# Performance work log

Measured on AMD Instinct MI355X. Metric: run time of the kernel, lower is better.

The kernel has to match this reference:

```python
import jax, jax.numpy as jnp
import numpy as np
from jax import lax
from jax.scipy.special import logsumexp

B, S, V, D, DFF, H, T, L = 64, 512, 30000, 128, 256, 4, 9, 2
HD = D // H


def setup_inputs() -> dict:
    key = jax.random.key(0)
    ks = jax.random.split(key, 12)
    sc = 0.02
    return {
        "sentences": jax.random.randint(ks[0], (B, S), 0, V, dtype=jnp.int32),
        "tags": jax.random.randint(ks[1], (B, S), 0, T, dtype=jnp.int32),
        "emb": jax.random.normal(ks[2], (V, D), jnp.float32) * sc,
        "Wqkv": jax.random.normal(ks[3], (L, 3 * D, D), jnp.float32) * sc,
        "bqkv": jnp.zeros((L, 3 * D), jnp.float32),
        "Wo": jax.random.normal(ks[4], (L, D, D), jnp.float32) * sc,
        "bo": jnp.zeros((L, D), jnp.float32),
        "W1": jax.random.normal(ks[5], (L, DFF, D), jnp.float32) * sc,
        "b1f": jnp.zeros((L, DFF), jnp.float32),
        "W2": jax.random.normal(ks[6], (L, D, DFF), jnp.float32) * sc,
        "b2f": jnp.zeros((L, D), jnp.float32),
        "ln1g": jnp.ones((L, D), jnp.float32), "ln1b": jnp.zeros((L, D), jnp.float32),
        "ln2g": jnp.ones((L, D), jnp.float32), "ln2b": jnp.zeros((L, D), jnp.float32),
        "Wtag": jax.random.normal(ks[7], (T, D), jnp.float32) * sc,
        "btag": jnp.zeros((T,), jnp.float32),
        "trans": jax.random.normal(ks[8], (T, T), jnp.float32) * 0.1,
        "start_t": jax.random.normal(ks[9], (T,), jnp.float32),
        "end_t": jax.random.normal(ks[10], (T,), jnp.float32),
    }


def _layernorm(x, g, b, eps=1e-5):
    mu = x.mean(-1, keepdims=True)
    var = ((x - mu) ** 2).mean(-1, keepdims=True)
    return (x - mu) / jnp.sqrt(var + eps) * g + b


def _forward_core(sentences, tags, emb, Wqkv, bqkv, Wo, bo, W1, b1f, W2, b2f,
                  ln1g, ln1b, ln2g, ln2b, Wtag, btag, trans, start_t, end_t):
    emb = emb.at[0].set(0.0)  # padding_idx=0
    mask = sentences != 0  # (B,S) key-padding mask (True = real token)
    x = emb[sentences]  # (B,S,D)
    # sinusoidal positional encoding (eval mode -> dropout is identity)
    pos = jnp.arange(S, dtype=jnp.float32)[:, None]
    div = jnp.exp(jnp.arange(0, D, 2, dtype=jnp.float32) * (-np.log(10000.0) / D))
    pe = jnp.zeros((S, D), jnp.float32).at[:, 0::2].set(jnp.sin(pos * div)).at[:, 1::2].set(jnp.cos(pos * div))
    x = x + pe[None]
    key_bias = jnp.where(mask, 0.0, -1e9)[:, None, None, :]  # (B,1,1,S)
    inv_sqrt_hd = 1.0 / np.sqrt(HD)
    for l in range(L):  # post-LN TransformerEncoderLayer, relu FFN
        qkv = x @ Wqkv[l].T + bqkv[l]
        q, k, v = jnp.split(qkv, 3, axis=-1)
        q = q.reshape(B, S, H, HD)
        k = k.reshape(B, S, H, HD)
        v = v.reshape(B, S, H, HD)
        scores = jnp.einsum('bqhd,bkhd->bhqk', q, k) * inv_sqrt_hd + key_bias
        attn = jax.nn.softmax(scores, axis=-1)
        ctx = jnp.einsum('bhqk,bkhd->bqhd', attn, v).reshape(B, S, D)
        x = _layernorm(x + ctx @ Wo[l].T + bo[l], ln1g[l], ln1b[l])
        ff = jax.nn.relu(x @ W1[l].T + b1f[l]) @ W2[l].T + b2f[l]
        x = _layernorm(x + ff, ln2g[l], ln2b[l])
    emissions = x @ Wtag.T + btag  # (B,S,T)

    # CRF forward algorithm (log-partition) as a scan over time
    fv0 = start_t[None, :] + emissions[:, 0]  # (B,T)

    def step(fv, xm):
        em_t, m_t = xm  # (B,T), (B,)
        nv = logsumexp(fv[:, :, None] + trans[None, :, :] + em_t[:, None, :], axis=1)
        return jnp.where(m_t[:, None], nv, fv), None

    fv, _ = lax.scan(step, fv0, (jnp.swapaxes(emissions[:, 1:], 0, 1),
                                 jnp.swapaxes(mask[:, 1:], 0, 1)))
    fwd_score = logsumexp(fv + end_t[None, :], axis=1)  # (B,)

    # gold path score (fully vectorized)
    bidx = jnp.arange(B)
    score = start_t[tags[:, 0]] + emissions[bidx, 0, tags[:, 0]]
    tprev, tcur = tags[:, :-1], tags[:, 1:]
    trans_sc = trans[tprev, tcur]  # (B,S-1)
    emit_sc = jnp.take_along_axis(emissions[:, 1:], tcur[:, :, None], axis=2)[:, :, 0]
    score = score + jnp.sum(jnp.where(mask[:, 1:], trans_sc + emit_sc, 0.0), axis=1)
    seq_lens = mask.sum(axis=1)
    last_tags = tags[bidx, seq_lens - 1]
    score = score + end_t[last_tags]

    return jnp.mean(fwd_score - score)


def reference(sentences, tags, emb, Wqkv, bqkv, Wo, bo, W1, b1f, W2, b2f,
              ln1g, ln1b, ln2g, ln2b, Wtag, btag, trans, start_t, end_t):
    return _forward_core(sentences, tags, emb, Wqkv, bqkv, Wo, bo, W1, b1f, W2, b2f,
                         ln1g, ln1b, ln2g, ln2b, Wtag, btag, trans, start_t, end_t)
```

## Files before the change

kernel.cpp:

```cpp
#include <hip/hip_runtime.h>

#define BB   64
#define SS   512
#define DD   128
#define DFFc 256
#define HH   4
#define TT   9
#define LL   2
#define HDc  32
#define NN   (BB*SS)

#define OFF_X    0
#define OFF_Y    (NN*DD)
#define OFF_QKV  (2*NN*DD)
#define OFF_CTX  (5*NN*DD)
#define OFF_KT   (6*NN*DD)
#define OFF_EM   (7*NN*DD)
#define OFF_PART (7*NN*DD + NN*TT)

typedef __attribute__((ext_vector_type(8))) short short8;
typedef __attribute__((ext_vector_type(8))) unsigned short ushort8;
typedef __attribute__((ext_vector_type(4))) float f32x4;

__device__ __forceinline__ unsigned short f2bf(float f) {
  unsigned int u = __float_as_uint(f);
  u += 0x7FFFu + ((u >> 16) & 1u);
  return (unsigned short)(u >> 16);
}
__device__ __forceinline__ float bf2f(unsigned short h) {
  return __uint_as_float(((unsigned int)h) << 16);
}

__global__ void k_embed(const int* __restrict__ sent, const float* __restrict__ emb,
                        float* __restrict__ x) {
  int n = blockIdx.x;
  int d = threadIdx.x;
  int tok = sent[n];
  int s = n & (SS - 1);
  float e = (tok != 0) ? emb[(size_t)tok * DD + d] : 0.f;
  int i = d >> 1;
  float dv = expf((float)(2 * i) * (-9.210340371976184f / (float)DD));
  float ang = (float)s * dv;
  float pe = (d & 1) ? cosf(ang) : sinf(ang);
  x[(size_t)n * DD + d] = e + pe;
}

template <int KTOT, bool RELU>
__global__ __launch_bounds__(256) void k_gemm(const float* __restrict__ X,
                                              const float* __restrict__ W,
                                              const float* __restrict__ bias,
                                              float* __restrict__ Y, int ldY) {
  __shared__ float Xs[64][68];
  __shared__ float Wt[64][68];
  const int tid = threadIdx.x;
  const int tx = tid & 15, ty = tid >> 4;
  const int n0 = blockIdx.x * 64, c0g = blockIdx.y * 64;
  float acc[4][4] = {};
  for (int kb = 0; kb < KTOT; kb += 64) {
    #pragma unroll
    for (int p = 0; p < 4; p++) {
      int r = p * 16 + (tid >> 4);
      int c4 = (tid & 15) * 4;
      *(float4*)&Xs[r][c4] = *(const float4*)&X[(size_t)(n0 + r) * KTOT + kb + c4];
    }
    #pragma unroll
    for (int p = 0; p < 4; p++) {
      int c = (tid >> 4) + 16 * p;
      int kk0 = tid & 15;
      #pragma unroll
      for (int ii = 0; ii < 4; ii++)
        Wt[kk0 + 16 * ii][c] = W[(size_t)(c0g + c) * KTOT + kb + kk0 + 16 * ii];
    }
    __syncthreads();
    #pragma unroll
    for (int k4 = 0; k4 < 16; k4++) {
      float4 a4[4], b4[4];
      #pragma unroll
      for (int i = 0; i < 4; i++) a4[i] = *(const float4*)&Xs[4 * ty + i][4 * k4];
      #pragma unroll
      for (int k = 0; k < 4; k++) b4[k] = *(const float4*)&Wt[4 * k4 + k][4 * tx];
      #pragma unroll
      for (int k = 0; k < 4; k++) {
        #pragma unroll
        for (int i = 0; i < 4; i++) {
          float av = (k == 0) ? a4[i].x : (k == 1) ? a4[i].y : (k == 2) ? a4[i].z : a4[i].w;
          acc[i][0] = fmaf(av, b4[k].x, acc[i][0]);
          acc[i][1] = fmaf(av, b4[k].y, acc[i][1]);
          acc[i][2] = fmaf(av, b4[k].z, acc[i][2]);
          acc[i][3] = fmaf(av, b4[k].w, acc[i][3]);
        }
      }
    }
    __syncthreads();
  }
  float4 bi = *(const float4*)&bias[c0g + 4 * tx];
  #pragma unroll
  for (int i = 0; i < 4; i++) {
    float4 o;
    o.x = acc[i][0] + bi.x; o.y = acc[i][1] + bi.y;
    o.z = acc[i][2] + bi.z; o.w = acc[i][3] + bi.w;
    if (RELU) {
      o.x = fmaxf(o.x, 0.f); o.y = fmaxf(o.y, 0.f);
      o.z = fmaxf(o.z, 0.f); o.w = fmaxf(o.w, 0.f);
    }
    *(float4*)&Y[(size_t)(n0 + 4 * ty + i) * ldY + c0g + 4 * tx] = o;
  }
}

template <int KTOT>
__global__ __launch_bounds__(256) void k_gemm_ln(const float* __restrict__ X,
                                                 const float* __restrict__ W,
                                                 const float* __restrict__ bias,
                                                 const float* __restrict__ Res,
                                                 const float* __restrict__ gam,
                                                 const float* __restrict__ bet,
                                                 float* __restrict__ Y) {
  __shared__ float Xs[32][68];
  __shared__ float Wt[64][132];
  const int tid = threadIdx.x;
  const int tx = tid & 31, ty = tid >> 5;
  const int n0 = blockIdx.x * 32;
  float acc[4][4] = {};
  for (int kb = 0; kb < KTOT; kb += 64) {
    #pragma unroll
    for (int p = 0; p < 2; p++) {
      int r = p * 16 + (tid >> 4);
      int c4 = (tid & 15) * 4;
      *(float4*)&Xs[r][c4] = *(const float4*)&X[(size_t)(n0 + r) * KTOT + kb + c4];
    }
    #pragma unroll
    for (int p = 0; p < 8; p++) {
      int c = (tid >> 4) + 16 * p;
      int kk0 = tid & 15;
      #pragma unroll
      for (int ii = 0; ii < 4; ii++)
        Wt[kk0 + 16 * ii][c] = W[(size_t)c * KTOT + kb + kk0 + 16 * ii];
    }
    __syncthreads();
    #pragma unroll
    for (int k4 = 0; k4 < 16; k4++) {
      float4 a4[4], b4[4];
      #pragma unroll
      for (int i = 0; i < 4; i++) a4[i] = *(const float4*)&Xs[4 * ty + i][4 * k4];
      #pragma unroll
      for (int k = 0; k < 4; k++) b4[k] = *(const float4*)&Wt[4 * k4 + k][4 * tx];
      #pragma unroll
      for (int k = 0; k < 4; k++) {
        #pragma unroll
        for (int i = 0; i < 4; i++) {
          float av = (k == 0) ? a4[i].x : (k == 1) ? a4[i].y : (k == 2) ? a4[i].z : a4[i].w;
          acc[i][0] = fmaf(av, b4[k].x, acc[i][0]);
          acc[i][1] = fmaf(av, b4[k].y, acc[i][1]);
          acc[i][2] = fmaf(av, b4[k].z, acc[i][2]);
          acc[i][3] = fmaf(av, b4[k].w, acc[i][3]);
        }
      }
    }
    __syncthreads();
  }
  const int c0 = 4 * tx;
  float4 bi = *(const float4*)&bias[c0];
  float4 gm = *(const float4*)&gam[c0];
  float4 be = *(const float4*)&bet[c0];
  #pragma unroll
  for (int i = 0; i < 4; i++) {
    int n = n0 + 4 * ty + i;
    float4 rs = *(const float4*)&Res[(size_t)n * DD + c0];
    float v0 = acc[i][0] + bi.x + rs.x;
    float v1 = acc[i][1] + bi.y + rs.y;
    float v2 = acc[i][2] + bi.z + rs.z;
    float v3 = acc[i][3] + bi.w + rs.w;
    float s1 = v0 + v1 + v2 + v3;
    float s2 = v0 * v0 + v1 * v1 + v2 * v2 + v3 * v3;
    #pragma unroll
    for (int off = 16; off >= 1; off >>= 1) {
      s1 += __shfl_xor(s1, off);
      s2 += __shfl_xor(s2, off);
    }
    float mu = s1 * 0.0078125f;
    float var = s2 * 0.0078125f - mu * mu;
    float rstd = rsqrtf(var + 1e-5f);
    float4 o;
    o.x = (v0 - mu) * rstd * gm.x + be.x;
    o.y = (v1 - mu) * rstd * gm.y + be.y;
    o.z = (v2 - mu) * rstd * gm.z + be.z;
    o.w = (v3 - mu) * rstd * gm.w + be.w;
    *(float4*)&Y[(size_t)n * DD + c0] = o;
  }
}

__global__ void k_pack(const float* __restrict__ qkv,
                       unsigned short* __restrict__ Kh, unsigned short* __restrict__ Kl,
                       unsigned short* __restrict__ Vh, unsigned short* __restrict__ Vl) {
  const int st = blockIdx.x * 64;
  const int bh = blockIdx.y;
  const int b = bh >> 2, h = bh & 3;
  const int tid = threadIdx.x;
  __shared__ float tile[64][33];
  #pragma unroll
  for (int p = 0; p < 8; p++) {
    int sl = p * 8 + (tid >> 5);
    int d = tid & 31;
    const float* src = qkv + (size_t)(b * SS + st + sl) * 384 + h * 32 + d;
    float kv = src[128];
    unsigned short khu = f2bf(kv);
    size_t o = (size_t)(bh * SS + st + sl) * 32 + d;
    Kh[o] = khu;
    Kl[o] = f2bf(kv - bf2f(khu));
    tile[sl][d] = src[256];
  }
  __syncthreads();
  int d = tid >> 3, s0 = (tid & 7) * 8;
  ushort8 vh, vl;
  #pragma unroll
  for (int i = 0; i < 8; i++) {
    float v = tile[s0 + i][d];
    unsigned short hu = f2bf(v);
    vh[i] = hu;
    vl[i] = f2bf(v - bf2f(hu));
  }
  size_t o = (size_t)(bh * 32 + d) * SS + st + s0;
  *(ushort8*)&Vh[o] = vh;
  *(ushort8*)&Vl[o] = vl;
}

__global__ __launch_bounds__(256) void k_attn(const float* __restrict__ qkv,
    const unsigned short* __restrict__ Kh, const unsigned short* __restrict__ Kl,
    const unsigned short* __restrict__ Vh, const unsigned short* __restrict__ Vl,
    const int* __restrict__ sent, float* __restrict__ ctx) {
  const int id = blockIdx.x;
  const int xcd = id & 7, rem = id >> 3;
  const int qt = rem & 7;
  const int bh = xcd + 8 * (rem >> 3);
  const int b = bh >> 2, h = bh & 3;
  const int tid = threadIdx.x, w = tid >> 6, lane = tid & 63;
  const int l15 = lane & 15, kg = lane >> 4;

  __shared__ float kb_lds[512];
  __shared__ unsigned short Ph[4][16][136];
  __shared__ unsigned short Pl[4][16][136];
  __shared__ float l_lds[4][16];

  for (int i = tid; i < 512; i += 256)
    kb_lds[i] = (sent[b * SS + i] != 0) ? 0.f : -1e9f;
  __syncthreads();

  const int qrow = qt * 64 + w * 16 + l15;
  const float* qp = qkv + (size_t)(b * SS + qrow) * 384 + h * 32 + kg * 8;
  short8 qh, ql;
  #pragma unroll
  for (int i = 0; i < 8; i++) {
    float v = qp[i];
    unsigned short hu = f2bf(v);
    qh[i] = (short)hu;
    ql[i] = (short)f2bf(v - bf2f(hu));
  }

  f32x4 acc0 = {0.f, 0.f, 0.f, 0.f};
  f32x4 acc1 = {0.f, 0.f, 0.f, 0.f};
  float ls[4] = {0.f, 0.f, 0.f, 0.f};
  const float scale = 0.17677669529663687f;

  const unsigned short* KhB = Kh + (size_t)bh * SS * 32;
  const unsigned short* KlB = Kl + (size_t)bh * SS * 32;
  const unsigned short* VhB = Vh + (size_t)bh * 32 * SS;
  const unsigned short* VlB = Vl + (size_t)bh * 32 * SS;

  for (int c = 0; c < 4; c++) {
    const int ksb = c * 128;
    f32x4 sc[8];
    #pragma unroll
    for (int t = 0; t < 8; t++) {
      size_t ko = (size_t)(ksb + t * 16 + l15) * 32 + kg * 8;
      short8 kh_ = *(const short8*)(KhB + ko);
      short8 kl_ = *(const short8*)(KlB + ko);
      f32x4 z = {0.f, 0.f, 0.f, 0.f};
      f32x4 s = __builtin_amdgcn_mfma_f32_16x16x32_bf16(qh, kh_, z, 0, 0, 0);
      s = __builtin_amdgcn_mfma_f32_16x16x32_bf16(qh, kl_, s, 0, 0, 0);
      s = __builtin_amdgcn_mfma_f32_16x16x32_bf16(ql, kh_, s, 0, 0, 0);
      sc[t] = s;
    }
    #pragma unroll
    for (int t = 0; t < 8; t++) {
      float kbv = kb_lds[ksb + t * 16 + l15];
      #pragma unroll
      for (int j = 0; j < 4; j++) {
        float s = fmaf(sc[t][j], scale, kbv);
        float p = __expf(s);
        ls[j] += p;
        unsigned short ph = f2bf(p);
        Ph[w][kg * 4 + j][t * 16 + l15] = ph;
        Pl[w][kg * 4 + j][t * 16 + l15] = f2bf(p - bf2f(ph));
      }
    }
    #pragma unroll
    for (int k4 = 0; k4 < 4; k4++) {
      short8 ph_ = *(const short8*)&Ph[w][l15][k4 * 32 + kg * 8];
      short8 pl_ = *(const short8*)&Pl[w][l15][k4 * 32 + kg * 8];
      size_t vo0 = (size_t)l15 * SS + ksb + k4 * 32 + kg * 8;
      size_t vo1 = (size_t)(16 + l15) * SS + ksb + k4 * 32 + kg * 8;
      short8 vh0 = *(const short8*)(VhB + vo0);
      short8 vl0 = *(const short8*)(VlB + vo0);
      acc0 = __builtin_amdgcn_mfma_f32_16x16x32_bf16(vh0, ph_, acc0, 0, 0, 0);
      acc0 = __builtin_amdgcn_mfma_f32_16x16x32_bf16(vh0, pl_, acc0, 0, 0, 0);
      acc0 = __builtin_amdgcn_mfma_f32_16x16x32_bf16(vl0, ph_, acc0, 0, 0, 0);
      short8 vh1 = *(const short8*)(VhB + vo1);
      short8 vl1 = *(const short8*)(VlB + vo1);
      acc1 = __builtin_amdgcn_mfma_f32_16x16x32_bf16(vh1, ph_, acc1, 0, 0, 0);
      acc1 = __builtin_amdgcn_mfma_f32_16x16x32_bf16(vh1, pl_, acc1, 0, 0, 0);
      acc1 = __builtin_amdgcn_mfma_f32_16x16x32_bf16(vl1, ph_, acc1, 0, 0, 0);
    }
  }
  #pragma unroll
  for (int j = 0; j < 4; j++) {
    #pragma unroll
    for (int off = 1; off <= 8; off <<= 1) ls[j] += __shfl_xor(ls[j], off);
  }
  if (l15 == 0) {
    #pragma unroll
    for (int j = 0; j < 4; j++) l_lds[w][kg * 4 + j] = ls[j];
  }
  float linv = 1.f / l_lds[w][l15];
  float* cp = ctx + (size_t)(b * SS + qrow) * DD + h * 32;
  #pragma unroll
  for (int j = 0; j < 4; j++) {
    cp[kg * 4 + j] = acc0[j] * linv;
    cp[16 + kg * 4 + j] = acc1[j] * linv;
  }
}

__global__ void k_emis(const float* __restrict__ X, const float* __restrict__ Wtag,
                       const float* __restrict__ btag, float* __restrict__ em) {
  int idx = blockIdx.x * 256 + threadIdx.x;
  if (idx >= NN * TT) return;
  int n = idx / TT, t = idx - n * TT;
  const float* xr = X + (size_t)n * DD;
  const float* wr = Wtag + (size_t)t * DD;
  float acc = 0.f;
  #pragma unroll
  for (int k = 0; k < DD / 4; k++) {
    float4 x4 = *(const float4*)(xr + 4 * k);
    float4 w4 = *(const float4*)(wr + 4 * k);
    acc += x4.x * w4.x + x4.y * w4.y + x4.z * w4.z + x4.w * w4.w;
  }
  em[idx] = acc + btag[t];
}

__global__ void k_crf_scan(const float* __restrict__ em, const int* __restrict__ sent,
                           const float* __restrict__ trans, float* __restrict__ M) {
  const int i = blockIdx.x;
  const int c = blockIdx.y;
  const int b = blockIdx.z;
  const int lane = threadIdx.x;
  const int j = (lane < TT) ? lane : 0;
  float tr[TT];
  #pragma unroll
  for (int k = 0; k < TT; k++) tr[k] = trans[k * TT + j];
  const float* emb_ = em + (size_t)b * SS * TT;
  float v = (j == i) ? 0.f : -1e30f;
  const int s0 = 1 + c * 64;
  const int s1 = (s0 + 64 < SS) ? s0 + 64 : SS;
  for (int s = s0; s < s1; s++) {
    int tok = sent[b * SS + s];
    if (tok != 0) {
      float a[TT];
      #pragma unroll
      for (int k = 0; k < TT; k++) a[k] = __shfl(v, k) + tr[k];
      float m = a[0];
      #pragma unroll
      for (int k = 1; k < TT; k++) m = fmaxf(m, a[k]);
      float sum = 0.f;
      #pragma unroll
      for (int k = 0; k < TT; k++) sum += __expf(a[k] - m);
      v = emb_[s * TT + j] + m + __logf(sum);
    }
  }
  if (lane < TT) M[(((size_t)b * 8 + c) * TT + i) * TT + j] = v;
}

__global__ void k_crf_comb(const float* __restrict__ em, const int* __restrict__ sent,
                           const int* __restrict__ tags, const float* __restrict__ trans,
                           const float* __restrict__ start_t, const float* __restrict__ end_t,
                           const float* __restrict__ M, float* __restrict__ part) {
  const int b = blockIdx.x;
  const int lane = threadIdx.x;
  const int j = (lane < TT) ? lane : 0;
  const float* emb_ = em + (size_t)b * SS * TT;
  float fv = start_t[j] + emb_[j];
  #pragma unroll
  for (int c = 0; c < 8; c++) {
    const float* Mc = M + (((size_t)b * 8 + c) * TT) * TT;
    float a[TT];
    #pragma unroll
    for (int k = 0; k < TT; k++) a[k] = __shfl(fv, k) + Mc[k * TT + j];
    float m = a[0];
    #pragma unroll
    for (int k = 1; k < TT; k++) m = fmaxf(m, a[k]);
    float sum = 0.f;
    #pragma unroll
    for (int k = 0; k < TT; k++) sum += __expf(a[k] - m);
    fv = m + __logf(sum);
  }
  float aa[TT];
  #pragma unroll
  for (int i = 0; i < TT; i++) aa[i] = __shfl(fv, i) + end_t[i];
  float m2 = aa[0];
  #pragma unroll
  for (int i = 1; i < TT; i++) m2 = fmaxf(m2, aa[i]);
  float sum2 = 0.f;
  #pragma unroll
  for (int i = 0; i < TT; i++) sum2 += __expf(aa[i] - m2);
  float fwd = m2 + __logf(sum2);
  float p = 0.f;
  int cnt = 0;
  #pragma unroll
  for (int ii = 0; ii < 8; ii++) {
    int s = lane + 64 * ii;
    cnt += (sent[b * SS + s] != 0) ? 1 : 0;
    int s2 = s + 1;
    if (s2 < SS && sent[b * SS + s2] != 0) {
      int tp = tags[b * SS + s2 - 1];
      int tc = tags[b * SS + s2];
      p += trans[tp * TT + tc] + emb_[(size_t)s2 * TT + tc];
    }
  }
  #pragma unroll
  for (int off = 32; off >= 1; off >>= 1) {
    p += __shfl_xor(p, off);
    cnt += __shfl_xor(cnt, off);
  }
  if (lane == 0) {
    int t0 = tags[b * SS];
    float score = start_t[t0] + emb_[t0] + p;
    int lastt = tags[b * SS + cnt - 1];
    score += end_t[lastt];
    part[b] = fwd - score;
  }
}

__global__ void k_final(const float* __restrict__ part, float* __restrict__ out) {
  float v = part[threadIdx.x];
  #pragma unroll
  for (int off = 32; off >= 1; off >>= 1) v += __shfl_xor(v, off);
  if (threadIdx.x == 0) out[0] = v * (1.f / 64.f);
}

extern "C" void kernel_launch(void* const* d_in, const int* in_sizes, int n_in,
                              void* d_out, int out_size, void* d_ws, size_t ws_size,
                              hipStream_t stream) {
  const int*   sent  = (const int*)d_in[0];
  const int*   tags  = (const int*)d_in[1];
  const float* emb   = (const float*)d_in[2];
  const float* Wqkv  = (const float*)d_in[3];
  const float* bqkv  = (const float*)d_in[4];
  const float* Wo    = (const float*)d_in[5];
  const float* bo    = (const float*)d_in[6];
  const float* W1    = (const float*)d_in[7];
  const float* b1f   = (const float*)d_in[8];
  const float* W2    = (const float*)d_in[9];
  const float* b2f   = (const float*)d_in[10];
  const float* ln1g  = (const float*)d_in[11];
  const float* ln1b  = (const float*)d_in[12];
  const float* ln2g  = (const float*)d_in[13];
  const float* ln2b  = (const float*)d_in[14];
  const float* Wtag  = (const float*)d_in[15];
  const float* btag  = (const float*)d_in[16];
  const float* trans = (const float*)d_in[17];
  const float* st    = (const float*)d_in[18];
  const float* et    = (const float*)d_in[19];

  float* ws   = (float*)d_ws;
  float* xA   = ws + OFF_X;
  float* xB   = ws + OFF_Y;
  float* qkv  = ws + OFF_QKV;
  float* ff   = ws + OFF_QKV;
  float* ctx  = ws + OFF_CTX;
  float* em   = ws + OFF_EM;
  float* part = ws + OFF_PART;
  float* out  = (float*)d_out;

  unsigned short* Kh = (unsigned short*)(ws + OFF_KT);
  unsigned short* Vh = Kh + (size_t)NN * DD;
  unsigned short* Kl = (unsigned short*)(ws + OFF_Y);
  unsigned short* Vl = Kl + (size_t)NN * DD;
  float* Mbuf = ws + OFF_CTX;

  k_embed<<<NN, DD, 0, stream>>>(sent, emb, xA);

  for (int l = 0; l < LL; l++) {
    k_gemm<128, false><<<dim3(NN / 64, 6), 256, 0, stream>>>(
        xA, Wqkv + (size_t)l * 3 * DD * DD, bqkv + l * 3 * DD, qkv, 3 * DD);
    k_pack<<<dim3(8, BB * HH), 256, 0, stream>>>(qkv, Kh, Kl, Vh, Vl);
    k_attn<<<dim3(2048), 256, 0, stream>>>(qkv, Kh, Kl, Vh, Vl, sent, ctx);
    k_gemm_ln<128><<<dim3(NN / 32), 256, 0, stream>>>(
        ctx, Wo + (size_t)l * DD * DD, bo + l * DD, xA, ln1g + l * DD, ln1b + l * DD, xB);
    k_gemm<128, true><<<dim3(NN / 64, 4), 256, 0, stream>>>(
        xB, W1 + (size_t)l * DFFc * DD, b1f + l * DFFc, ff, DFFc);
    k_gemm_ln<256><<<dim3(NN / 32), 256, 0, stream>>>(
        ff, W2 + (size_t)l * DD * DFFc, b2f + l * DD, xB, ln2g + l * DD, ln2b + l * DD, xA);
  }

  k_emis<<<(NN * TT + 255) / 256, 256, 0, stream>>>(xA, Wtag, btag, em);
  k_crf_scan<<<dim3(TT, 8, BB), 64, 0, stream>>>(em, sent, trans, Mbuf);
  k_crf_comb<<<BB, 64, 0, stream>>>(em, sent, tags, trans, st, et, Mbuf, part);
  k_final<<<1, 64, 0, stream>>>(part, out);
}
```

Baseline: 675.5 us.

## Move dense GEMMs to split-bf16 MFMA with packed hi/lo activations

Result: slower. 735.5 us (+8.9%).

```diff
diff --git a/kernel.cpp b/kernel.cpp
--- a/kernel.cpp
+++ b/kernel.cpp
@@ -32,7 +32,8 @@
 }
 
 __global__ void k_embed(const int* __restrict__ sent, const float* __restrict__ emb,
-                        float* __restrict__ x) {
+                        float* __restrict__ x,
+                        unsigned short* __restrict__ xh, unsigned short* __restrict__ xl) {
   int n = blockIdx.x;
   int d = threadIdx.x;
   int tok = sent[n];
@@ -42,150 +43,144 @@
   float dv = expf((float)(2 * i) * (-9.210340371976184f / (float)DD));
   float ang = (float)s * dv;
   float pe = (d & 1) ? cosf(ang) : sinf(ang);
-  x[(size_t)n * DD + d] = e + pe;
-}
-
-template <int KTOT, bool RELU>
-__global__ __launch_bounds__(256) void k_gemm(const float* __restrict__ X,
-                                              const float* __restrict__ W,
-                                              const float* __restrict__ bias,
-                                              float* __restrict__ Y, int ldY) {
-  __shared__ float Xs[64][68];
-  __shared__ float Wt[64][68];
-  const int tid = threadIdx.x;
-  const int tx = tid & 15, ty = tid >> 4;
-  const int n0 = blockIdx.x * 64, c0g = blockIdx.y * 64;
-  float acc[4][4] = {};
-  for (int kb = 0; kb < KTOT; kb += 64) {
-    #pragma unroll
-    for (int p = 0; p < 4; p++) {
-      int r = p * 16 + (tid >> 4);
-      int c4 = (tid & 15) * 4;
-      *(float4*)&Xs[r][c4] = *(const float4*)&X[(size_t)(n0 + r) * KTOT + kb + c4];
-    }
-    #pragma unroll
-    for (int p = 0; p < 4; p++) {
-      int c = (tid >> 4) + 16 * p;
-      int kk0 = tid & 15;
-      #pragma unroll
-      for (int ii = 0; ii < 4; ii++)
-        Wt[kk0 + 16 * ii][c] = W[(size_t)(c0g + c) * KTOT + kb + kk0 + 16 * ii];
-    }
-    __syncthreads();
-    #pragma unroll
-    for (int k4 = 0; k4 < 16; k4++) {
-      float4 a4[4], b4[4];
-      #pragma unroll
-      for (int i = 0; i < 4; i++) a4[i] = *(const float4*)&Xs[4 * ty + i][4 * k4];
-      #pragma unroll
-      for (int k = 0; k < 4; k++) b4[k] = *(const float4*)&Wt[4 * k4 + k][4 * tx];
-      #pragma unroll
-      for (int k = 0; k < 4; k++) {
-        #pragma unroll
-        for (int i = 0; i < 4; i++) {
-          float av = (k == 0) ? a4[i].x : (k == 1) ? a4[i].y : (k == 2) ? a4[i].z : a4[i].w;
-          acc[i][0] = fmaf(av, b4[k].x, acc[i][0]);
-          acc[i][1] = fmaf(av, b4[k].y, acc[i][1]);
-          acc[i][2] = fmaf(av, b4[k].z, acc[i][2]);
-          acc[i][3] = fmaf(av, b4[k].w, acc[i][3]);
-        }
+  float v = e + pe;
+  size_t o = (size_t)n * DD + d;
+  x[o] = v;
+  unsigned short h = f2bf(v);
+  xh[o] = h;
+  xl[o] = f2bf(v - bf2f(h));
+}
+
+__global__ void k_packw(const float* __restrict__ Wqkv, const float* __restrict__ Wo,
+                        const float* __restrict__ W1, const float* __restrict__ W2,
+                        unsigned short* __restrict__ Wh, unsigned short* __restrict__ Wl) {
+  int idx = (blockIdx.x * 256 + threadIdx.x) * 4;
+  const float* src;
+  int off;
+  if (idx < 49152)      { src = Wqkv; off = idx; }
+  else if (idx < 65536) { src = Wo;   off = idx - 49152; }
+  else if (idx < 98304) { src = W1;   off = idx - 65536; }
+  else                  { src = W2;   off = idx - 98304; }
+  float4 v = *(const float4*)(src + off);
+  unsigned short h0 = f2bf(v.x), h1 = f2bf(v.y), h2 = f2bf(v.z), h3 = f2bf(v.w);
+  Wh[idx + 0] = h0; Wh[idx + 1] = h1; Wh[idx + 2] = h2; Wh[idx + 3] = h3;
+  Wl[idx + 0] = f2bf(v.x - bf2f(h0));
+  Wl[idx + 1] = f2bf(v.y - bf2f(h1));
+  Wl[idx + 2] = f2bf(v.z - bf2f(h2));
+  Wl[idx + 3] = f2bf(v.w - bf2f(h3));
+}
+
+template <int KTOT, bool RELU, bool PACKOUT>
+__global__ __launch_bounds__(256) void k_bgemm(
+    const unsigned short* __restrict__ Xh, const unsigned short* __restrict__ Xl,
+    const unsigned short* __restrict__ Wh, const unsigned short* __restrict__ Wl,
+    const float* __restrict__ bias, float* __restrict__ Y, int ldY,
+    unsigned short* __restrict__ Yh, unsigned short* __restrict__ Yl,
+    int ncb) {
+  const int id = blockIdx.x;
+  const int cb = id % ncb, rb = id / ncb;
+  const int tid = threadIdx.x, w = tid >> 6, lane = tid & 63;
+  const int l15 = lane & 15, kg = lane >> 4;
+  const int n0 = rb * 64 + w * 16;
+  const int c0 = cb * 64;
+  f32x4 acc[4] = {};
+  const unsigned short* xph = Xh + (size_t)(n0 + l15) * KTOT + kg * 8;
+  const unsigned short* xpl = Xl + (size_t)(n0 + l15) * KTOT + kg * 8;
+  #pragma unroll
+  for (int ks = 0; ks < KTOT / 32; ks++) {
+    short8 ah = *(const short8*)(xph + ks * 32);
+    short8 al = *(const short8*)(xpl + ks * 32);
+    #pragma unroll
+    for (int ct = 0; ct < 4; ct++) {
+      size_t wo = (size_t)(c0 + ct * 16 + l15) * KTOT + ks * 32 + kg * 8;
+      short8 bh = *(const short8*)(Wh + wo);
+      short8 bl = *(const short8*)(Wl + wo);
+      acc[ct] = __builtin_amdgcn_mfma_f32_16x16x32_bf16(ah, bh, acc[ct], 0, 0, 0);
+      acc[ct] = __builtin_amdgcn_mfma_f32_16x16x32_bf16(ah, bl, acc[ct], 0, 0, 0);
+      acc[ct] = __builtin_amdgcn_mfma_f32_16x16x32_bf16(al, bh, acc[ct], 0, 0, 0);
+    }
+  }
+  #pragma unroll
+  for (int ct = 0; ct < 4; ct++) {
+    int c = c0 + ct * 16 + l15;
+    float bi = bias[c];
+    #pragma unroll
+    for (int j = 0; j < 4; j++) {
+      float v = acc[ct][j] + bi;
+      if (RELU) v = fmaxf(v, 0.f);
+      int n = n0 + kg * 4 + j;
+      if (PACKOUT) {
+        unsigned short h = f2bf(v);
+        Yh[(size_t)n * ldY + c] = h;
+        Yl[(size_t)n * ldY + c] = f2bf(v - bf2f(h));
+      } else {
+        Y[(size_t)n * ldY + c] = v;
       }
     }
-    __syncthreads();
-  }
-  float4 bi = *(const float4*)&bias[c0g + 4 * tx];
-  #pragma unroll
-  for (int i = 0; i < 4; i++) {
-    float4 o;
-    o.x = acc[i][0] + bi.x; o.y = acc[i][1] + bi.y;
-    o.z = acc[i][2] + bi.z; o.w = acc[i][3] + bi.w;
-    if (RELU) {
-      o.x = fmaxf(o.x, 0.f); o.y = fmaxf(o.y, 0.f);
-      o.z = fmaxf(o.z, 0.f); o.w = fmaxf(o.w, 0.f);
-    }
-    *(float4*)&Y[(size_t)(n0 + 4 * ty + i) * ldY + c0g + 4 * tx] = o;
   }
 }
 
 template <int KTOT>
-__global__ __launch_bounds__(256) void k_gemm_ln(const float* __restrict__ X,
-                                                 const float* __restrict__ W,
-                                                 const float* __restrict__ bias,
-                                                 const float* __restrict__ Res,
-                                                 const float* __restrict__ gam,
-                                                 const float* __restrict__ bet,
-                                                 float* __restrict__ Y) {
-  __shared__ float Xs[32][68];
-  __shared__ float Wt[64][132];
-  const int tid = threadIdx.x;
-  const int tx = tid & 31, ty = tid >> 5;
-  const int n0 = blockIdx.x * 32;
-  float acc[4][4] = {};
-  for (int kb = 0; kb < KTOT; kb += 64) {
-    #pragma unroll
-    for (int p = 0; p < 2; p++) {
-      int r = p * 16 + (tid >> 4);
-      int c4 = (tid & 15) * 4;
-      *(float4*)&Xs[r][c4] = *(const float4*)&X[(size_t)(n0 + r) * KTOT + kb + c4];
-    }
-    #pragma unroll
-    for (int p = 0; p < 8; p++) {
-      int c = (tid >> 4) + 16 * p;
-      int kk0 = tid & 15;
-      #pragma unroll
-      for (int ii = 0; ii < 4; ii++)
-        Wt[kk0 + 16 * ii][c] = W[(size_t)c * KTOT + kb + kk0 + 16 * ii];
-    }
-    __syncthreads();
-    #pragma unroll
-    for (int k4 = 0; k4 < 16; k4++) {
-      float4 a4[4], b4[4];
-      #pragma unroll
-      for (int i = 0; i < 4; i++) a4[i] = *(const float4*)&Xs[4 * ty + i][4 * k4];
-      #pragma unroll
-      for (int k = 0; k < 4; k++) b4[k] = *(const float4*)&Wt[4 * k4 + k][4 * tx];
-      #pragma unroll
-      for (int k = 0; k < 4; k++) {
-        #pragma unroll
-        for (int i = 0; i < 4; i++) {
-          float av = (k == 0) ? a4[i].x : (k == 1) ? a4[i].y : (k == 2) ? a4[i].z : a4[i].w;
-          acc[i][0] = fmaf(av, b4[k].x, acc[i][0]);
-          acc[i][1] = fmaf(av, b4[k].y, acc[i][1]);
-          acc[i][2] = fmaf(av, b4[k].z, acc[i][2]);
-          acc[i][3] = fmaf(av, b4[k].w, acc[i][3]);
-        }
-      }
-    }
-    __syncthreads();
-  }
-  const int c0 = 4 * tx;
-  float4 bi = *(const float4*)&bias[c0];
-  float4 gm = *(const float4*)&gam[c0];
-  float4 be = *(const float4*)&bet[c0];
-  #pragma unroll
-  for (int i = 0; i < 4; i++) {
-    int n = n0 + 4 * ty + i;
-    float4 rs = *(const float4*)&Res[(size_t)n * DD + c0];
-    float v0 = acc[i][0] + bi.x + rs.x;
-    float v1 = acc[i][1] + bi.y + rs.y;
-    float v2 = acc[i][2] + bi.z + rs.z;
-    float v3 = acc[i][3] + bi.w + rs.w;
-    float s1 = v0 + v1 + v2 + v3;
-    float s2 = v0 * v0 + v1 * v1 + v2 * v2 + v3 * v3;
-    #pragma unroll
-    for (int off = 16; off >= 1; off >>= 1) {
+__global__ __launch_bounds__(256) void k_bgemm_ln(
+    const unsigned short* __restrict__ Xh, const unsigned short* __restrict__ Xl,
+    const unsigned short* __restrict__ Wh, const unsigned short* __restrict__ Wl,
+    const float* __restrict__ bias, const float* __restrict__ Res,
+    const float* __restrict__ gam, const float* __restrict__ bet,
+    float* __restrict__ Y,
+    unsigned short* __restrict__ Yh, unsigned short* __restrict__ Yl,
+    int dopack) {
+  const int tid = threadIdx.x, w = tid >> 6, lane = tid & 63;
+  const int l15 = lane & 15, kg = lane >> 4;
+  const int n0 = blockIdx.x * 64 + w * 16;
+  f32x4 acc[8] = {};
+  const unsigned short* xph = Xh + (size_t)(n0 + l15) * KTOT + kg * 8;
+  const unsigned short* xpl = Xl + (size_t)(n0 + l15) * KTOT + kg * 8;
+  #pragma unroll
+  for (int ks = 0; ks < KTOT / 32; ks++) {
+    short8 ah = *(const short8*)(xph + ks * 32);
+    short8 al = *(const short8*)(xpl + ks * 32);
+    #pragma unroll
+    for (int ct = 0; ct < 8; ct++) {
+      size_t wo = (size_t)(ct * 16 + l15) * KTOT + ks * 32 + kg * 8;
+      short8 bh = *(const short8*)(Wh + wo);
+      short8 bl = *(const short8*)(Wl + wo);
+      acc[ct] = __builtin_amdgcn_mfma_f32_16x16x32_bf16(ah, bh, acc[ct], 0, 0, 0);
+      acc[ct] = __builtin_amdgcn_mfma_f32_16x16x32_bf16(ah, bl, acc[ct], 0, 0, 0);
+      acc[ct] = __builtin_amdgcn_mfma_f32_16x16x32_bf16(al, bh, acc[ct], 0, 0, 0);
+    }
+  }
+  #pragma unroll
+  for (int j = 0; j < 4; j++) {
+    int n = n0 + kg * 4 + j;
+    float v[8], s1 = 0.f, s2 = 0.f;
+    #pragma unroll
+    for (int ct = 0; ct < 8; ct++) {
+      int c = ct * 16 + l15;
+      float t = acc[ct][j] + bias[c] + Res[(size_t)n * DD + c];
+      v[ct] = t;
+      s1 += t;
+      s2 += t * t;
+    }
+    #pragma unroll
+    for (int off = 1; off <= 8; off <<= 1) {
       s1 += __shfl_xor(s1, off);
       s2 += __shfl_xor(s2, off);
     }
     float mu = s1 * 0.0078125f;
     float var = s2 * 0.0078125f - mu * mu;
     float rstd = rsqrtf(var + 1e-5f);
-    float4 o;
-    o.x = (v0 - mu) * rstd * gm.x + be.x;
-    o.y = (v1 - mu) * rstd * gm.y + be.y;
-    o.z = (v2 - mu) * rstd * gm.z + be.z;
-    o.w = (v3 - mu) * rstd * gm.w + be.w;
-    *(float4*)&Y[(size_t)n * DD + c0] = o;
+    #pragma unroll
+    for (int ct = 0; ct < 8; ct++) {
+      int c = ct * 16 + l15;
+      float o = (v[ct] - mu) * rstd * gam[c] + bet[c];
+      size_t oo = (size_t)n * DD + c;
+      Y[oo] = o;
+      if (dopack) {
+        unsigned short h = f2bf(o);
+        Yh[oo] = h;
+        Yl[oo] = f2bf(o - bf2f(h));
+      }
+    }
   }
 }
 
@@ -227,7 +222,8 @@
 __global__ __launch_bounds__(256) void k_attn(const float* __restrict__ qkv,
     const unsigned short* __restrict__ Kh, const unsigned short* __restrict__ Kl,
     const unsigned short* __restrict__ Vh, const unsigned short* __restrict__ Vl,
-    const int* __restrict__ sent, float* __restrict__ ctx) {
+    const int* __restrict__ sent,
+    unsigned short* __restrict__ ctxh, unsigned short* __restrict__ ctxl) {
   const int id = blockIdx.x;
   const int xcd = id & 7, rem = id >> 3;
   const int qt = rem & 7;
@@ -321,11 +317,16 @@
     for (int j = 0; j < 4; j++) l_lds[w][kg * 4 + j] = ls[j];
   }
   float linv = 1.f / l_lds[w][l15];
-  float* cp = ctx + (size_t)(b * SS + qrow) * DD + h * 32;
+  size_t co = (size_t)(b * SS + qrow) * DD + h * 32;
   #pragma unroll
   for (int j = 0; j < 4; j++) {
-    cp[kg * 4 + j] = acc0[j] * linv;
-    cp[16 + kg * 4 + j] = acc1[j] * linv;
+    float v0 = acc0[j] * linv;
+    float v1 = acc1[j] * linv;
+    unsigned short h0 = f2bf(v0), h1 = f2bf(v1);
+    ctxh[co + kg * 4 + j] = h0;
+    ctxl[co + kg * 4 + j] = f2bf(v0 - bf2f(h0));
+    ctxh[co + 16 + kg * 4 + j] = h1;
+    ctxl[co + 16 + kg * 4 + j] = f2bf(v1 - bf2f(h1));
   }
 }
 
@@ -473,31 +474,46 @@
   float* xA   = ws + OFF_X;
   float* xB   = ws + OFF_Y;
   float* qkv  = ws + OFF_QKV;
-  float* ff   = ws + OFF_QKV;
-  float* ctx  = ws + OFF_CTX;
   float* em   = ws + OFF_EM;
   float* part = ws + OFF_PART;
   float* out  = (float*)d_out;
 
-  unsigned short* Kh = (unsigned short*)(ws + OFF_KT);
-  unsigned short* Vh = Kh + (size_t)NN * DD;
-  unsigned short* Kl = (unsigned short*)(ws + OFF_Y);
-  unsigned short* Vl = Kl + (size_t)NN * DD;
+  unsigned short* XAh  = (unsigned short*)(ws + OFF_CTX);
+  unsigned short* XAl  = XAh + (size_t)NN * DD;
+  unsigned short* ctxh = XAh;
+  unsigned short* ctxl = XAl;
+  unsigned short* Kh   = (unsigned short*)(ws + OFF_KT);
+  unsigned short* Vh   = Kh + (size_t)NN * DD;
+  unsigned short* Kl   = (unsigned short*)(ws + OFF_Y);
+  unsigned short* Vl   = Kl + (size_t)NN * DD;
+  unsigned short* xBh  = (unsigned short*)(ws + OFF_KT);
+  unsigned short* xBl  = xBh + (size_t)NN * DD;
+  unsigned short* ffh  = (unsigned short*)(ws + OFF_QKV);
+  unsigned short* ffl  = ffh + (size_t)NN * DFFc;
+  unsigned short* Wph  = (unsigned short*)(ws + OFF_EM);
+  unsigned short* Wpl  = Wph + 131072;
   float* Mbuf = ws + OFF_CTX;
 
-  k_embed<<<NN, DD, 0, stream>>>(sent, emb, xA);
+  k_embed<<<NN, DD, 0, stream>>>(sent, emb, xA, XAh, XAl);
 
   for (int l = 0; l < LL; l++) {
-    k_gemm<128, false><<<dim3(NN / 64, 6), 256, 0, stream>>>(
-        xA, Wqkv + (size_t)l * 3 * DD * DD, bqkv + l * 3 * DD, qkv, 3 * DD);
+    k_packw<<<128, 256, 0, stream>>>(Wqkv + (size_t)l * 3 * DD * DD,
+                                     Wo + (size_t)l * DD * DD,
+                                     W1 + (size_t)l * DFFc * DD,
+                                     W2 + (size_t)l * DD * DFFc, Wph, Wpl);
+    k_bgemm<128, false, false><<<dim3((NN / 64) * 6), 256, 0, stream>>>(
+        XAh, XAl, Wph, Wpl, bqkv + l * 3 * DD, qkv, 3 * DD, nullptr, nullptr, 6);
     k_pack<<<dim3(8, BB * HH), 256, 0, stream>>>(qkv, Kh, Kl, Vh, Vl);
-    k_attn<<<dim3(2048), 256, 0, stream>>>(qkv, Kh, Kl, Vh, Vl, sent, ctx);
-    k_gemm_ln<128><<<dim3(NN / 32), 256, 0, stream>>>(
-        ctx, Wo + (size_t)l * DD * DD, bo + l * DD, xA, ln1g + l * DD, ln1b + l * DD, xB);
-    k_gemm<128, true><<<dim3(NN / 64, 4), 256, 0, stream>>>(
-        xB, W1 + (size_t)l * DFFc * DD, b1f + l * DFFc, ff, DFFc);
-    k_gemm_ln<256><<<dim3(NN / 32), 256, 0, stream>>>(
-        ff, W2 + (size_t)l * DD * DFFc, b2f + l * DD, xB, ln2g + l * DD, ln2b + l * DD, xA);
+    k_attn<<<dim3(2048), 256, 0, stream>>>(qkv, Kh, Kl, Vh, Vl, sent, ctxh, ctxl);
+    k_bgemm_ln<128><<<dim3(NN / 64), 256, 0, stream>>>(
+        ctxh, ctxl, Wph + 49152, Wpl + 49152, bo + l * DD, xA,
+        ln1g + l * DD, ln1b + l * DD, xB, xBh, xBl, 1);
+    k_bgemm<128, true, true><<<dim3((NN / 64) * 4), 256, 0, stream>>>(
+        xBh, xBl, Wph + 65536, Wpl + 65536, b1f + l * DFFc, nullptr, DFFc,
+        ffh, ffl, 4);
+    k_bgemm_ln<256><<<dim3(NN / 64), 256, 0, stream>>>(
+        ffh, ffl, Wph + 98304, Wpl + 98304, b2f + l * DD, xB,
+        ln2g + l * DD, ln2b + l * DD, xA, XAh, XAl, (l + 1 < LL) ? 1 : 0);
   }
 
   k_emis<<<(NN * TT + 255) / 256, 256, 0, stream>>>(xA, Wtag, btag, em);
```
